# Optimization experiments

Measured on AMD Instinct MI355X. Metric: run time of the kernel, lower is better.

The kernel has to match this reference:

```python
import jax, jax.numpy as jnp
import numpy as np

WIN = (7, 7, 7)
DIM = 192
HEADS = 6
N = WIN[0] * WIN[1] * WIN[2]  # 343
TABLE = (2 * WIN[0] - 1) * (2 * WIN[1] - 1) * (2 * WIN[2] - 1)  # 2197


def _relative_position_index():
    d, h, w = WIN
    coords = np.stack(np.meshgrid(np.arange(d), np.arange(h), np.arange(w), indexing='ij'))
    flat = coords.reshape(3, -1)  # [3, N]
    rel = flat[:, :, None] - flat[:, None, :]  # [3, N, N]
    rel = rel.transpose(1, 2, 0).copy()
    rel[:, :, 0] += d - 1
    rel[:, :, 1] += h - 1
    rel[:, :, 2] += w - 1
    rel[:, :, 0] *= (2 * h - 1) * (2 * w - 1)
    rel[:, :, 1] *= 2 * w - 1
    return jnp.asarray(rel.sum(-1), dtype=jnp.int32)  # [N, N]


def setup_inputs() -> dict:
    key = jax.random.key(0)
    ks = jax.random.split(key, 8)
    b = 256
    nw = 64
    x = jax.random.normal(ks[0], (b, N, DIM), dtype=jnp.float32)
    mask = jax.random.normal(ks[1], (nw, N, N), dtype=jnp.float32)
    s = 1.0 / np.sqrt(DIM)
    wq = jax.random.normal(ks[2], (DIM, DIM), dtype=jnp.float32) * s
    wk = jax.random.normal(ks[3], (DIM, DIM), dtype=jnp.float32) * s
    wv = jax.random.normal(ks[4], (DIM, DIM), dtype=jnp.float32) * s
    rel_table = jax.random.normal(ks[5], (TABLE, HEADS), dtype=jnp.float32) * 0.02
    proj_w = jax.random.normal(ks[6], (DIM, DIM), dtype=jnp.float32) * s
    proj_b = jnp.zeros((DIM,), dtype=jnp.float32)
    return {"x": x, "mask": mask, "wq": wq, "wk": wk, "wv": wv,
            "rel_table": rel_table, "proj_w": proj_w, "proj_b": proj_b}


def reference(x, mask, wq, wk, wv, rel_table, proj_w, proj_b):
    b, n, c = x.shape
    hd = c // HEADS
    scale = hd ** (-0.5)
    rel_idx = _relative_position_index()[:n, :n]  # [n, n] int32
    # torch Linear: x @ W.T  -> [b, H, n, hd]
    q = (x @ wq.T).reshape(b, n, HEADS, hd).transpose(0, 2, 1, 3) * scale
    k = (x @ wk.T).reshape(b, n, HEADS, hd).transpose(0, 2, 1, 3)
    v = (x @ wv.T).reshape(b, n, HEADS, hd).transpose(0, 2, 1, 3)
    attn = jnp.einsum('bhqd,bhkd->bhqk', q, k)  # [b, H, n, n]
    bias = rel_table[rel_idx.reshape(-1)].reshape(n, n, HEADS)
    attn = attn + bias.transpose(2, 0, 1)[None]
    nw = mask.shape[0]
    attn = attn.reshape(b // nw, nw, HEADS, n, n) + mask[None, :, None]
    attn = attn.reshape(b, HEADS, n, n)
    attn = jax.nn.softmax(attn, axis=-1)
    out = jnp.einsum('bhqk,bhkd->bhqd', attn, v).transpose(0, 2, 1, 3).reshape(b, n, c)
    return out @ proj_w.T + proj_b
```

## Files before the change

### kernel.cpp

```cpp
#include <hip/hip_runtime.h>
#include <hip/hip_bf16.h>

typedef __bf16 bf16_t;
typedef __bf16 bf16x8 __attribute__((ext_vector_type(8)));
typedef float f32x4 __attribute__((ext_vector_type(4)));

#define N_TOK 343
#define NP    352
#define DIM   192
#define HEADS 6
#define HD    32
#define BATCH 256
#define NW    64
#define MROWS (BATCH * N_TOK)
#define LOG2E 1.4426950408889634f

static __device__ __forceinline__ f32x4 mfma_bf16(bf16x8 a, bf16x8 b, f32x4 c) {
    return __builtin_amdgcn_mfma_f32_16x16x32_bf16(a, b, c, 0, 0, 0);
}

__global__ __launch_bounds__(256) void wprep_kernel(
    const float* __restrict__ wq, const float* __restrict__ wk,
    const float* __restrict__ wv, const float* __restrict__ pw,
    bf16_t* __restrict__ wb)
{
    int t = blockIdx.x * 256 + threadIdx.x;
    int mat = t / 4608, off = (t % 4608) * 8;
    const float* src = (mat == 0) ? wq : ((mat == 1) ? wk : ((mat == 2) ? wv : pw));
    const float scale = (mat == 0) ? (0.17677669529663687f * LOG2E) : 1.0f;
    float4 f0 = *(const float4*)(src + off);
    float4 f1 = *(const float4*)(src + off + 4);
    bf16x8 o;
    o[0]=(bf16_t)(f0.x*scale); o[1]=(bf16_t)(f0.y*scale);
    o[2]=(bf16_t)(f0.z*scale); o[3]=(bf16_t)(f0.w*scale);
    o[4]=(bf16_t)(f1.x*scale); o[5]=(bf16_t)(f1.y*scale);
    o[6]=(bf16_t)(f1.z*scale); o[7]=(bf16_t)(f1.w*scale);
    *(bf16x8*)(wb + mat * 36864 + off) = o;
}

__global__ __launch_bounds__(256) void qkv_kernel(
    const float* __restrict__ x, const bf16_t* __restrict__ wb,
    bf16_t* __restrict__ qo, bf16_t* __restrict__ ko, bf16_t* __restrict__ vo)
{
    __shared__ __align__(16) bf16_t xs[64 * 200];
    const int tid = threadIdx.x;
    const long m0 = (long)blockIdx.x * 64;
    for (int e = tid; e < 3072; e += 256) {
        int flat = e * 4;
        int row = flat / 192, col = flat - row * 192;
        float4 f = *(const float4*)(x + m0 * 192 + flat);
        bf16_t* dst = &xs[row * 200 + col];
        dst[0] = (bf16_t)f.x; dst[1] = (bf16_t)f.y;
        dst[2] = (bf16_t)f.z; dst[3] = (bf16_t)f.w;
    }
    __syncthreads();
    const int wave = tid >> 6, lane = tid & 63;
    const int g = lane >> 4, c = lane & 15;
    #pragma unroll 1
    for (int ct = wave; ct < 36; ct += 4) {
        const int mat = ct / 12, n0 = (ct % 12) * 16;
        bf16_t* O = (mat == 0) ? qo : ((mat == 1) ? ko : vo);
        const bf16_t* wrow = wb + mat * 36864 + (n0 + c) * 192 + g * 8;
        bf16x8 bfrag[6];
        #pragma unroll
        for (int ks = 0; ks < 6; ks++) bfrag[ks] = *(const bf16x8*)(wrow + ks * 32);
        #pragma unroll
        for (int mt = 0; mt < 4; mt++) {
            f32x4 acc = {0.f, 0.f, 0.f, 0.f};
            #pragma unroll
            for (int ks = 0; ks < 6; ks++) {
                bf16x8 a = *(const bf16x8*)&xs[(mt * 16 + c) * 200 + ks * 32 + g * 8];
                acc = mfma_bf16(a, bfrag[ks], acc);
            }
            long mb = m0 + mt * 16 + g * 4;
            #pragma unroll
            for (int i = 0; i < 4; i++)
                O[(mb + i) * 192 + n0 + c] = (bf16_t)acc[i];
        }
    }
}

__global__ void maskprep_kernel(const float* __restrict__ mask, bf16_t* __restrict__ mp) {
    long row = blockIdx.x;
    int t = threadIdx.x;
    if (t < NP) {
        float vv = (t < N_TOK) ? mask[row * N_TOK + t] * LOG2E : -1e30f;
        mp[row * NP + t] = (bf16_t)vv;
    }
}

__global__ void biasprep_kernel(const float* __restrict__ rel_table, bf16_t* __restrict__ bp) {
    int r = blockIdx.x;
    int h = blockIdx.y;
    int j = threadIdx.x;
    if (j < NP) {
        float vv = 0.f;
        if (j < N_TOK) {
            int dr = r / 49, hr = (r / 7) % 7, wr = r % 7;
            int dj = j / 49, hj = (j / 7) % 7, wj = j % 7;
            int idx = (dr - dj + 6) * 169 + (hr - hj + 6) * 13 + (wr - wj + 6);
            vv = rel_table[idx * HEADS + h] * LOG2E;
        }
        bp[((long)h * N_TOK + r) * NP + j] = (bf16_t)vv;
    }
}

__global__ __launch_bounds__(256) void attn_kernel(
    const bf16_t* __restrict__ q, const bf16_t* __restrict__ k,
    const bf16_t* __restrict__ v, const bf16_t* __restrict__ maskp,
    const bf16_t* __restrict__ biasp, bf16_t* __restrict__ aout)
{
    __shared__ __align__(16) bf16_t K_lds[NP * 40];
    __shared__ __align__(16) bf16_t Vt_lds[HD * 360];
    const int b = blockIdx.x, h = blockIdx.y;
    const int tid = threadIdx.x;
    const bf16_t* kbase = k + (long)b * N_TOK * DIM + h * HD;
    const bf16_t* vbase = v + (long)b * N_TOK * DIM + h * HD;
    const bf16_t* qb    = q + (long)b * N_TOK * DIM + h * HD;

    for (int idx = tid; idx < 1408; idx += 256) {
        int j = idx >> 2, dcol = (idx & 3) * 8;
        int blk = j >> 5, w32 = j & 31;
        int gg = w32 >> 3, rem = w32 & 7, tt = rem >> 2, ii = rem & 3;
        int lr = blk * 32 + tt * 16 + gg * 4 + ii;
        bf16x8 val = {};
        if (j < N_TOK) val = *(const bf16x8*)(kbase + (long)j * DIM + dcol);
        *(bf16x8*)&K_lds[lr * 40 + dcol] = val;
    }
    for (int idx = tid; idx < 1408; idx += 256) {
        int j = idx >> 2, dcol = (idx & 3) * 8;
        if (j < N_TOK) {
            bf16x8 val = *(const bf16x8*)(vbase + (long)j * DIM + dcol);
            #pragma unroll
            for (int ii = 0; ii < 8; ii++) Vt_lds[(dcol + ii) * 360 + j] = val[ii];
        } else {
            #pragma unroll
            for (int ii = 0; ii < 8; ii++) Vt_lds[(dcol + ii) * 360 + j] = (bf16_t)0.f;
        }
    }
    __syncthreads();

    const int wave = tid >> 6, lane = tid & 63;
    const int g = lane >> 4, c = lane & 15;
    const bf16_t* mbase = maskp + (long)(b & 63) * N_TOK * NP;
    const bf16_t* bbase = biasp + (long)h * N_TOK * NP;

    for (int qt = wave; qt < 22; qt += 4) {
        const int rc = min(qt * 16 + c, N_TOK - 1);
        bf16x8 qf = *(const bf16x8*)(qb + (long)rc * DIM + g * 8);
        const bf16_t* mrow = mbase + (long)rc * NP;
        const bf16_t* brow = bbase + (long)rc * NP;
        f32x4 olo = {0.f,0.f,0.f,0.f}, ohi = {0.f,0.f,0.f,0.f};
        float rs = 0.f;
        for (int jb = 0; jb < 11; jb++) {
            const int j0 = jb * 32 + g * 8;
            bf16x8 mk = *(const bf16x8*)(mrow + j0);
            bf16x8 bk = *(const bf16x8*)(brow + j0);
            f32x4 c0, c1;
            #pragma unroll
            for (int e = 0; e < 4; e++) {
                c0[e] = (float)mk[e]     + (float)bk[e];
                c1[e] = (float)mk[4 + e] + (float)bk[4 + e];
            }
            bf16x8 k0 = *(const bf16x8*)&K_lds[(jb * 32 + c) * 40 + g * 8];
            bf16x8 k1 = *(const bf16x8*)&K_lds[(jb * 32 + 16 + c) * 40 + g * 8];
            f32x4 s0 = mfma_bf16(k0, qf, c0);
            f32x4 s1 = mfma_bf16(k1, qf, c1);
            float p[8];
            #pragma unroll
            for (int e = 0; e < 4; e++) {
                p[e]     = __builtin_amdgcn_exp2f(s0[e]);
                p[4 + e] = __builtin_amdgcn_exp2f(s1[e]);
            }
            #pragma unroll
            for (int e = 0; e < 8; e++) rs += p[e];
            bf16x8 pf;
            #pragma unroll
            for (int e = 0; e < 8; e++) pf[e] = (bf16_t)p[e];
            bf16x8 v0 = *(const bf16x8*)&Vt_lds[c * 360 + j0];
            bf16x8 v1 = *(const bf16x8*)&Vt_lds[(c + 16) * 360 + j0];
            olo = mfma_bf16(pf, v0, olo);
            ohi = mfma_bf16(pf, v1, ohi);
        }
        rs += __shfl_xor(rs, 16);
        rs += __shfl_xor(rs, 32);
        #pragma unroll
        for (int i = 0; i < 4; i++) {
            int row = qt * 16 + g * 4 + i;
            if (row < N_TOK) {
                float inv = 1.f / __shfl(rs, g * 4 + i);
                bf16_t* dst = aout + ((long)b * N_TOK + row) * DIM + h * HD;
                dst[c]      = (bf16_t)(olo[i] * inv);
                dst[c + 16] = (bf16_t)(ohi[i] * inv);
            }
        }
    }
}

__global__ __launch_bounds__(256) void proj_kernel(
    const bf16_t* __restrict__ A, const bf16_t* __restrict__ wb,
    const float* __restrict__ bias, float* __restrict__ out)
{
    __shared__ __align__(16) bf16_t xs[64 * 200];
    const int tid = threadIdx.x;
    const long m0 = (long)blockIdx.x * 64;
    for (int e = tid; e < 1536; e += 256) {
        int row = e / 24, col = (e % 24) * 8;
        *(bf16x8*)&xs[row * 200 + col] = *(const bf16x8*)(A + (m0 + row) * 192 + col);
    }
    __syncthreads();
    const int wave = tid >> 6, lane = tid & 63;
    const int g = lane >> 4, c = lane & 15;
    #pragma unroll 1
    for (int ct = wave; ct < 12; ct += 4) {
        const int n0 = ct * 16;
        const bf16_t* wrow = wb + 3 * 36864 + (n0 + c) * 192 + g * 8;
        bf16x8 bfrag[6];
        #pragma unroll
        for (int ks = 0; ks < 6; ks++) bfrag[ks] = *(const bf16x8*)(wrow + ks * 32);
        const float bv = bias[n0 + c];
        #pragma unroll
        for (int mt = 0; mt < 4; mt++) {
            f32x4 acc = {0.f, 0.f, 0.f, 0.f};
            #pragma unroll
            for (int ks = 0; ks < 6; ks++) {
                bf16x8 a = *(const bf16x8*)&xs[(mt * 16 + c) * 200 + ks * 32 + g * 8];
                acc = mfma_bf16(a, bfrag[ks], acc);
            }
            long mb = m0 + mt * 16 + g * 4;
            #pragma unroll
            for (int i = 0; i < 4; i++)
                out[(mb + i) * 192 + n0 + c] = acc[i] + bv;
        }
    }
}

extern "C" void kernel_launch(void* const* d_in, const int* in_sizes, int n_in,
                              void* d_out, int out_size, void* d_ws, size_t ws_size,
                              hipStream_t stream)
{
    const float* x         = (const float*)d_in[0];
    const float* mask      = (const float*)d_in[1];
    const float* wq        = (const float*)d_in[2];
    const float* wk        = (const float*)d_in[3];
    const float* wv        = (const float*)d_in[4];
    const float* rel_table = (const float*)d_in[5];
    const float* proj_w    = (const float*)d_in[6];
    const float* proj_b    = (const float*)d_in[7];
    float* out = (float*)d_out;

    char* ws = (char*)d_ws;
    const size_t SZ = (size_t)MROWS * DIM * 2;
    bf16_t* q_ws  = (bf16_t*)(ws);
    bf16_t* k_ws  = (bf16_t*)(ws + SZ);
    bf16_t* v_ws  = (bf16_t*)(ws + 2 * SZ);
    bf16_t* a_ws  = (bf16_t*)(ws + 3 * SZ);
    bf16_t* mp_ws = (bf16_t*)(ws + 4 * SZ);
    bf16_t* bp_ws = (bf16_t*)(ws + 4 * SZ + (size_t)NW * N_TOK * NP * 2);
    bf16_t* wb_ws = (bf16_t*)(ws + 4 * SZ + (size_t)NW * N_TOK * NP * 2
                                 + (size_t)HEADS * N_TOK * NP * 2);

    hipLaunchKernelGGL(wprep_kernel, dim3(72), dim3(256), 0, stream,
                       wq, wk, wv, proj_w, wb_ws);
    hipLaunchKernelGGL(maskprep_kernel, dim3(NW * N_TOK), dim3(384), 0, stream, mask, mp_ws);
    hipLaunchKernelGGL(biasprep_kernel, dim3(N_TOK, HEADS), dim3(384), 0, stream,
                       rel_table, bp_ws);
    hipLaunchKernelGGL(qkv_kernel, dim3(1372), dim3(256), 0, stream,
                       x, wb_ws, q_ws, k_ws, v_ws);
    hipLaunchKernelGGL(attn_kernel, dim3(BATCH, HEADS), dim3(256), 0, stream,
                       q_ws, k_ws, v_ws, mp_ws, bp_ws, a_ws);
    hipLaunchKernelGGL(proj_kernel, dim3(1372), dim3(256), 0, stream,
                       a_ws, wb_ws, proj_b, out);
}
```

Before: 243.4 us.

## Store Q/K/V and attention output head-major and remap attention blocks per XCD

The QKV projection now writes Q, K and V as [batch, head, token, 32] instead of token-major rows of 192. Each attention block can then load its K/V/Q slice contiguously, and the attention output is read back through the same head-major layout by the projection kernel. The attention grid is flattened and remapped so blocks sharing a mask window and head land on the same XCD, which should improve L2 reuse of the mask and bias tiles. The cost is scattered 2-byte stores in the QKV epilogue and a divide by 343 per element in both GEMM kernels.

```diff
diff --git a/kernel.cpp b/kernel.cpp
--- a/kernel.cpp
+++ b/kernel.cpp
@@ -60,6 +60,7 @@
     for (int ct = wave; ct < 36; ct += 4) {
         const int mat = ct / 12, n0 = (ct % 12) * 16;
         bf16_t* O = (mat == 0) ? qo : ((mat == 1) ? ko : vo);
+        const int hh = n0 >> 5, dd = (n0 & 31) + c;
         const bf16_t* wrow = wb + mat * 36864 + (n0 + c) * 192 + g * 8;
         bf16x8 bfrag[6];
         #pragma unroll
@@ -72,10 +73,14 @@
                 bf16x8 a = *(const bf16x8*)&xs[(mt * 16 + c) * 200 + ks * 32 + g * 8];
                 acc = mfma_bf16(a, bfrag[ks], acc);
             }
-            long mb = m0 + mt * 16 + g * 4;
-            #pragma unroll
-            for (int i = 0; i < 4; i++)
-                O[(mb + i) * 192 + n0 + c] = (bf16_t)acc[i];
+            int mb = (int)m0 + mt * 16 + g * 4;
+            #pragma unroll
+            for (int i = 0; i < 4; i++) {
+                int m = mb + i;
+                int bb = m / 343;
+                int tok = m - bb * 343;
+                O[((long)(bb * 6 + hh) * 343 + tok) * 32 + dd] = (bf16_t)acc[i];
+            }
         }
     }
 }
@@ -112,11 +117,17 @@
 {
     __shared__ __align__(16) bf16_t K_lds[NP * 40];
     __shared__ __align__(16) bf16_t Vt_lds[HD * 360];
-    const int b = blockIdx.x, h = blockIdx.y;
+    const int f = blockIdx.x;
+    const int xcd = f & 7;
+    const int idx8 = f >> 3;
+    const int pair = xcd * 48 + (idx8 >> 2);
+    const int rep  = idx8 & 3;
+    const int w = pair / 6, h = pair - (pair / 6) * 6;
+    const int b = rep * 64 + w;
     const int tid = threadIdx.x;
-    const bf16_t* kbase = k + (long)b * N_TOK * DIM + h * HD;
-    const bf16_t* vbase = v + (long)b * N_TOK * DIM + h * HD;
-    const bf16_t* qb    = q + (long)b * N_TOK * DIM + h * HD;
+    const bf16_t* kbase = k + (long)(b * 6 + h) * N_TOK * HD;
+    const bf16_t* vbase = v + (long)(b * 6 + h) * N_TOK * HD;
+    const bf16_t* qb    = q + (long)(b * 6 + h) * N_TOK * HD;
 
     for (int idx = tid; idx < 1408; idx += 256) {
         int j = idx >> 2, dcol = (idx & 3) * 8;
@@ -124,13 +135,13 @@
         int gg = w32 >> 3, rem = w32 & 7, tt = rem >> 2, ii = rem & 3;
         int lr = blk * 32 + tt * 16 + gg * 4 + ii;
         bf16x8 val = {};
-        if (j < N_TOK) val = *(const bf16x8*)(kbase + (long)j * DIM + dcol);
+        if (j < N_TOK) val = *(const bf16x8*)(kbase + idx * 8);
         *(bf16x8*)&K_lds[lr * 40 + dcol] = val;
     }
     for (int idx = tid; idx < 1408; idx += 256) {
         int j = idx >> 2, dcol = (idx & 3) * 8;
         if (j < N_TOK) {
-            bf16x8 val = *(const bf16x8*)(vbase + (long)j * DIM + dcol);
+            bf16x8 val = *(const bf16x8*)(vbase + idx * 8);
             #pragma unroll
             for (int ii = 0; ii < 8; ii++) Vt_lds[(dcol + ii) * 360 + j] = val[ii];
         } else {
@@ -142,12 +153,12 @@
 
     const int wave = tid >> 6, lane = tid & 63;
     const int g = lane >> 4, c = lane & 15;
-    const bf16_t* mbase = maskp + (long)(b & 63) * N_TOK * NP;
+    const bf16_t* mbase = maskp + (long)w * N_TOK * NP;
     const bf16_t* bbase = biasp + (long)h * N_TOK * NP;
 
     for (int qt = wave; qt < 22; qt += 4) {
         const int rc = min(qt * 16 + c, N_TOK - 1);
-        bf16x8 qf = *(const bf16x8*)(qb + (long)rc * DIM + g * 8);
+        bf16x8 qf = *(const bf16x8*)(qb + (long)rc * HD + g * 8);
         const bf16_t* mrow = mbase + (long)rc * NP;
         const bf16_t* brow = bbase + (long)rc * NP;
         f32x4 olo = {0.f,0.f,0.f,0.f}, ohi = {0.f,0.f,0.f,0.f};
@@ -189,7 +200,7 @@
             int row = qt * 16 + g * 4 + i;
             if (row < N_TOK) {
                 float inv = 1.f / __shfl(rs, g * 4 + i);
-                bf16_t* dst = aout + ((long)b * N_TOK + row) * DIM + h * HD;
+                bf16_t* dst = aout + ((long)(b * 6 + h) * N_TOK + row) * HD;
                 dst[c]      = (bf16_t)(olo[i] * inv);
                 dst[c + 16] = (bf16_t)(ohi[i] * inv);
             }
@@ -206,7 +217,12 @@
     const long m0 = (long)blockIdx.x * 64;
     for (int e = tid; e < 1536; e += 256) {
         int row = e / 24, col = (e % 24) * 8;
-        *(bf16x8*)&xs[row * 200 + col] = *(const bf16x8*)(A + (m0 + row) * 192 + col);
+        int m = (int)m0 + row;
+        int bb = m / 343;
+        int tok = m - bb * 343;
+        int hh = col >> 5, dd = col & 31;
+        *(bf16x8*)&xs[row * 200 + col] =
+            *(const bf16x8*)(A + ((long)(bb * 6 + hh) * 343 + tok) * 32 + dd);
     }
     __syncthreads();
     const int wave = tid >> 6, lane = tid & 63;
@@ -267,7 +283,7 @@
                        rel_table, bp_ws);
     hipLaunchKernelGGL(qkv_kernel, dim3(1372), dim3(256), 0, stream,
                        x, wb_ws, q_ws, k_ws, v_ws);
-    hipLaunchKernelGGL(attn_kernel, dim3(BATCH, HEADS), dim3(256), 0, stream,
+    hipLaunchKernelGGL(attn_kernel, dim3(BATCH * HEADS), dim3(256), 0, stream,
                        q_ws, k_ws, v_ws, mp_ws, bp_ws, a_ws);
     hipLaunchKernelGGL(proj_kernel, dim3(1372), dim3(256), 0, stream,
                        a_ws, wb_ws, proj_b, out);
```

Result: no change. 245.1 us (+0.7%).
